# Performance work log

Measured on AMD Instinct MI355X. Metric: run time of the kernel, lower is better.

The kernel has to match this reference:

```python
import jax, jax.numpy as jnp
import numpy as np

D_MODEL = 1024
D_HEAD = 64
N_HEADS = D_MODEL // D_HEAD
MAX_SEQ = 2048
BATCH = 2
SEQ = 2048


def setup_inputs() -> dict:
    key = jax.random.key(0)
    ks = jax.random.split(key, 10)
    s = 1.0 / np.sqrt(D_MODEL)
    return {
        "x": jax.random.normal(ks[0], (BATCH, SEQ, D_MODEL), dtype=jnp.float32),
        "Wq": jax.random.normal(ks[1], (D_MODEL, D_MODEL), dtype=jnp.float32) * s,
        "bq": jax.random.normal(ks[2], (D_MODEL,), dtype=jnp.float32) * 0.01,
        "Wk": jax.random.normal(ks[3], (D_MODEL, D_MODEL), dtype=jnp.float32) * s,
        "bk": jax.random.normal(ks[4], (D_MODEL,), dtype=jnp.float32) * 0.01,
        "Wv": jax.random.normal(ks[5], (D_MODEL, D_MODEL), dtype=jnp.float32) * s,
        "bv": jax.random.normal(ks[6], (D_MODEL,), dtype=jnp.float32) * 0.01,
        "Er": jax.random.normal(ks[7], (MAX_SEQ, D_HEAD), dtype=jnp.float32),
        "Wo": jax.random.normal(ks[8], (D_MODEL, D_MODEL), dtype=jnp.float32) * s,
        "bo": jax.random.normal(ks[9], (D_MODEL,), dtype=jnp.float32) * 0.01,
    }


def _s_rel(q, Er):
    # q: [B,H,S,Dh]; use last S rows of Er (start = max_seq - seq)
    S = q.shape[2]
    Er_slice = Er[Er.shape[0] - S:, :]                  # [S, Dh]
    qE = jnp.einsum("bhsd,ld->bhsl", q, Er_slice)       # [B,H,S,S]
    padded = jnp.pad(qE, ((0, 0), (0, 0), (0, 0), (1, 0)))  # [B,H,S,S+1]
    B, H, S1, S2 = padded.shape
    padded = padded.reshape(B, H, S2, S1)               # skew trick
    return padded[:, :, 1:, :]                          # [B,H,S,S]


def reference(x, Wq, bq, Wk, bk, Wv, bv, Er, Wo, bo):
    B, S, _ = x.shape
    scale = 1.0 / np.sqrt(D_HEAD)
    # projections (torch Linear: x @ W.T + b)
    def proj(W, b):
        return (x @ W.T + b).reshape(B, S, N_HEADS, D_HEAD).transpose(0, 2, 1, 3)
    q = proj(Wq, bq)   # [B,H,S,Dh]
    k = proj(Wk, bk)
    v = proj(Wv, bv)
    qk = jnp.einsum("bhsd,bhtd->bhst", q, k)            # [B,H,S,S]
    logits = (qk + _s_rel(q, Er)) * scale
    causal = jnp.tril(jnp.ones((S, S), dtype=bool))
    masked = jnp.where(causal[None, None], logits, -1e9)
    attn = jax.nn.softmax(masked, axis=-1)
    out = jnp.einsum("bhst,bhtd->bhsd", attn, v)        # [B,H,S,Dh]
    out = out.transpose(0, 2, 1, 3).reshape(B, S, D_MODEL)
    return out @ Wo.T + bo
```

## Files before the change

### kernel.cpp

```cpp
#include <hip/hip_runtime.h>
#include <hip/hip_bf16.h>

typedef short v8s __attribute__((ext_vector_type(8)));
typedef float v4f __attribute__((ext_vector_type(4)));
typedef __hip_bfloat16 bf16;
typedef unsigned int u32;

#define MFMA(a, b, c) __builtin_amdgcn_mfma_f32_16x16x32_bf16(a, b, c, 0, 0, 0)

__device__ __forceinline__ void gload16(const bf16* g, bf16* l) {
    __builtin_amdgcn_global_load_lds(
        (const __attribute__((address_space(1))) u32*)(g),
        (__attribute__((address_space(3))) u32*)(l), 16, 0, 0);
}

__global__ __launch_bounds__(256) void cast_all(
    const float* __restrict__ x,  const float* __restrict__ wq,
    const float* __restrict__ wk, const float* __restrict__ wv,
    const float* __restrict__ wo, const float* __restrict__ er,
    bf16* __restrict__ xb,  bf16* __restrict__ wqb, bf16* __restrict__ wkb,
    bf16* __restrict__ wvb, bf16* __restrict__ wob, bf16* __restrict__ erb)
{
    const int r = blockIdx.y;
    const float* s; bf16* d; int n4;
    if      (r == 0) { s = x;  d = xb;  n4 = 1048576; }
    else if (r == 1) { s = wq; d = wqb; n4 = 262144;  }
    else if (r == 2) { s = wk; d = wkb; n4 = 262144;  }
    else if (r == 3) { s = wv; d = wvb; n4 = 262144;  }
    else if (r == 4) { s = wo; d = wob; n4 = 262144;  }
    else             { s = er; d = erb; n4 = 32768;   }
    const int i = blockIdx.x * 256 + threadIdx.x;
    if (i < n4) {
        const float4 v = ((const float4*)s)[i];
        bf16 t[4];
        t[0] = __float2bfloat16(v.x);
        t[1] = __float2bfloat16(v.y);
        t[2] = __float2bfloat16(v.z);
        t[3] = __float2bfloat16(v.w);
        ((uint2*)d)[i] = *(const uint2*)t;
    }
}

__global__ __launch_bounds__(256) void gemm_nt(
    const bf16* __restrict__ A, const bf16* __restrict__ W,
    const float* __restrict__ b0, const float* __restrict__ b1,
    const float* __restrict__ b2,
    bf16* __restrict__ oHM, bf16* __restrict__ Vt, float* __restrict__ outf)
{
    __shared__ bf16 As[128 * 64];
    __shared__ bf16 Bs[128 * 64];

    const int tid = threadIdx.x;
    const int w  = tid >> 6, l = tid & 63;
    const int lm = l & 15,  lq = l >> 4;
    const int wm = (w >> 1) * 64, wn = (w & 1) * 64;
    const int m0 = blockIdx.y * 128, n0 = blockIdx.x * 128;

    const int grow = l >> 3;
    const int gcol = ((l & 7) ^ grow) * 8;

    v4f acc[4][4];
#pragma unroll
    for (int i = 0; i < 4; ++i)
#pragma unroll
        for (int j = 0; j < 4; ++j) acc[i][j] = (v4f){0.f, 0.f, 0.f, 0.f};

    const int sw = (lm & 7) << 4;

    for (int k0 = 0; k0 < 1024; k0 += 64) {
        __syncthreads();
#pragma unroll
        for (int q = 0; q < 4; ++q) {
            const int rr = w * 32 + q * 8;
            gload16(&A[(size_t)(m0 + rr + grow) * 1024 + k0 + gcol], &As[rr * 64]);
            gload16(&W[(size_t)(n0 + rr + grow) * 1024 + k0 + gcol], &Bs[rr * 64]);
        }
        __syncthreads();
#pragma unroll
        for (int kk = 0; kk < 2; ++kk) {
            v8s a[4], b[4];
            const int cb = (lq * 16 + kk * 64);
#pragma unroll
            for (int i = 0; i < 4; ++i) {
                const int row = wm + i * 16 + lm;
                a[i] = *(const v8s*)((const char*)As + row * 128 + (cb ^ sw));
            }
#pragma unroll
            for (int j = 0; j < 4; ++j) {
                const int row = wn + j * 16 + lm;
                b[j] = *(const v8s*)((const char*)Bs + row * 128 + (cb ^ sw));
            }
#pragma unroll
            for (int i = 0; i < 4; ++i)
#pragma unroll
                for (int j = 0; j < 4; ++j)
                    acc[i][j] = MFMA(b[j], a[i], acc[i][j]);
        }
    }

    const int z = blockIdx.x >> 3;
    const float* bias = (z == 0) ? b0 : (z == 1) ? b1 : b2;

    float4 bj[4];
#pragma unroll
    for (int j = 0; j < 4; ++j)
        bj[j] = *(const float4*)&bias[(n0 & 1023) + wn + j * 16 + lq * 4];

#pragma unroll
    for (int i = 0; i < 4; ++i) {
        const int row = m0 + wm + i * 16 + lm;
        const int bb = row >> 11, ss = row & 2047;
#pragma unroll
        for (int j = 0; j < 4; ++j) {
            const int cc = (n0 & 1023) + wn + j * 16 + lq * 4;
            const float v0 = acc[i][j][0] + bj[j].x;
            const float v1 = acc[i][j][1] + bj[j].y;
            const float v2 = acc[i][j][2] + bj[j].z;
            const float v3 = acc[i][j][3] + bj[j].w;
            if (outf) {
                const float4 fv = {v0, v1, v2, v3};
                *(float4*)&outf[(size_t)row * 1024 + cc] = fv;
            } else {
                bf16 t[4];
                t[0] = __float2bfloat16(v0);
                t[1] = __float2bfloat16(v1);
                t[2] = __float2bfloat16(v2);
                t[3] = __float2bfloat16(v3);
                const int hh = cc >> 6, dd = cc & 63;
                if (z < 2) {
                    *(uint2*)&oHM[(size_t)z * 4194304 +
                        ((size_t)(bb * 16 + hh) * 2048 + ss) * 64 + dd] = *(uint2*)t;
                } else {
#pragma unroll
                    for (int r = 0; r < 4; ++r)
                        Vt[((size_t)(bb * 16 + hh) * 64 + dd + r) * 2048 + ss] = t[r];
                }
            }
        }
    }
}

__global__ __launch_bounds__(256, 5) void attn(
    const bf16* __restrict__ Q, const bf16* __restrict__ K,
    const bf16* __restrict__ Vt, const bf16* __restrict__ Er,
    bf16* __restrict__ AO, float* __restrict__ Opart, float* __restrict__ dpart)
{
    __shared__ bf16 Ks[64 * 72];
    __shared__ bf16 Vs[64 * 72];
    __shared__ bf16 GPs[64 * 84];

    const int ord = blockIdx.x;
    int bh, qb, t0, t1, slot = -1;
    if (ord < 960) {
        qb = 31 - (ord >> 6);
        const int sub = ord & 63;
        bh = sub >> 1;
        const int half = sub & 1;
        const int hh2 = (qb + 1) >> 1;
        t0 = half ? hh2 : 0;
        t1 = half ? (qb + 1) : hh2;
        slot = ((31 - qb) * 32 + bh) * 2 + half;
    } else {
        const int g2 = ord - 960;
        qb = 16 - (g2 >> 5);
        bh = g2 & 31;
        t0 = 0; t1 = qb + 1;
    }

    const int i0 = qb * 64;
    const int b  = bh >> 4, h = bh & 15;
    const int tid = threadIdx.x;
    const int w  = tid >> 6, l = tid & 63;
    const int lm = l & 15,  lq = l >> 4;

    const bf16* qp = Q + ((size_t)bh * 2048 + i0 + w * 16 + lm) * 64 + lq * 8;
    const v8s q0 = *(const v8s*)qp;
    const v8s q1f = *(const v8s*)(qp + 32);

    v4f accO[4];
#pragma unroll
    for (int dt = 0; dt < 4; ++dt) accO[dt] = (v4f){0.f, 0.f, 0.f, 0.f};
    float rs[4];
#pragma unroll
    for (int r = 0; r < 4; ++r) rs[r] = 0.f;

    const int sr0 = tid >> 3;
    const int sc8 = (tid & 7) * 8;
    const size_t kbase = (size_t)bh * 2048 * 64;
    const size_t vbase = (size_t)bh * 64 * 2048;

    const int jt0 = t0 * 64;
    uint4 kp0 = *(const uint4*)&K[kbase + (size_t)(jt0 + sr0) * 64 + sc8];
    uint4 kp1 = *(const uint4*)&K[kbase + (size_t)(jt0 + sr0 + 32) * 64 + sc8];
    uint4 vp0 = *(const uint4*)&Vt[vbase + (size_t)sr0 * 2048 + jt0 + sc8];
    uint4 vp1 = *(const uint4*)&Vt[vbase + (size_t)(sr0 + 32) * 2048 + jt0 + sc8];

    for (int it = t0; it < t1; ++it) {
        const int j0 = it * 64;
        __syncthreads();
        *(uint4*)&Ks[sr0 * 72 + sc8]        = kp0;
        *(uint4*)&Ks[(sr0 + 32) * 72 + sc8] = kp1;
        *(uint4*)&Vs[sr0 * 72 + sc8]        = vp0;
        *(uint4*)&Vs[(sr0 + 32) * 72 + sc8] = vp1;
        if (it + 1 < t1) {
            const int jn = j0 + 64;
            kp0 = *(const uint4*)&K[kbase + (size_t)(jn + sr0) * 64 + sc8];
            kp1 = *(const uint4*)&K[kbase + (size_t)(jn + sr0 + 32) * 64 + sc8];
            vp0 = *(const uint4*)&Vt[vbase + (size_t)sr0 * 2048 + jn + sc8];
            vp1 = *(const uint4*)&Vt[vbase + (size_t)(sr0 + 32) * 2048 + jn + sc8];
        }
        const int basew = 2048 - 16 - i0 + j0 - 16 * w;
#pragma unroll
        for (int ct2 = 0; ct2 < 5; ++ct2) {
            int mr = basew + ct2 * 16 + lm;
            mr = (mr > 2047) ? 2047 : mr;
            const bf16* ep = Er + (size_t)mr * 64 + lq * 8;
            const v8s e0 = *(const v8s*)ep;
            const v8s e1 = *(const v8s*)(ep + 32);
            v4f g = (v4f){0.f, 0.f, 0.f, 0.f};
            g = MFMA(q0, e0, g);
            g = MFMA(q1f, e1, g);
#pragma unroll
            for (int r = 0; r < 4; ++r)
                GPs[(w * 16 + lq * 4 + r) * 84 + ct2 * 16 + lm] =
                    __float2bfloat16(g[r] * 0.125f);
        }
        __syncthreads();
        v4f sv[4];
#pragma unroll
        for (int ct = 0; ct < 4; ++ct) {
            const v8s k0f = *(const v8s*)&Ks[(ct * 16 + lm) * 72 + lq * 8];
            const v8s k1f = *(const v8s*)&Ks[(ct * 16 + lm) * 72 + 32 + lq * 8];
            v4f s = (v4f){0.f, 0.f, 0.f, 0.f};
            s = MFMA(q0, k0f, s);
            s = MFMA(q1f, k1f, s);
            sv[ct] = s;
        }
#pragma unroll
        for (int r = 0; r < 4; ++r) {
            const int rl = lq * 4 + r;
            const int ig = i0 + w * 16 + rl;
#pragma unroll
            for (int ct = 0; ct < 4; ++ct) {
                const int jj = ct * 16 + lm;
                const float gb = (float)GPs[(w * 16 + rl) * 84 + jj + 15 - rl];
                float s = fmaf(sv[ct][r], 0.125f, gb);
                if (j0 + jj > ig) s = -1e9f;
                const float pe = __expf(s - 4.0f);
                rs[r] += pe;
                GPs[(w * 16 + rl) * 84 + jj] = __float2bfloat16(pe);
            }
        }
        const v8s pa0 = *(const v8s*)&GPs[(w * 16 + lm) * 84 + lq * 8];
        const v8s pa1 = *(const v8s*)&GPs[(w * 16 + lm) * 84 + 32 + lq * 8];
#pragma unroll
        for (int dt = 0; dt < 4; ++dt) {
            const v8s vb0 = *(const v8s*)&Vs[(dt * 16 + lm) * 72 + lq * 8];
            const v8s vb1 = *(const v8s*)&Vs[(dt * 16 + lm) * 72 + 32 + lq * 8];
            accO[dt] = MFMA(pa0, vb0, accO[dt]);
            accO[dt] = MFMA(pa1, vb1, accO[dt]);
        }
    }
#pragma unroll
    for (int r = 0; r < 4; ++r) {
#pragma unroll
        for (int msk = 8; msk >= 1; msk >>= 1)
            rs[r] += __shfl_xor(rs[r], msk, 64);
    }
    if (slot < 0) {
#pragma unroll
        for (int dt = 0; dt < 4; ++dt) {
#pragma unroll
            for (int r = 0; r < 4; ++r) {
                const int row = i0 + w * 16 + lq * 4 + r;
                const int d   = dt * 16 + lm;
                const float v = accO[dt][r] / rs[r];
                AO[((size_t)b * 2048 + row) * 1024 + h * 64 + d] = __float2bfloat16(v);
            }
        }
    } else {
        float* op = Opart + (size_t)slot * 4096;
#pragma unroll
        for (int dt = 0; dt < 4; ++dt) {
#pragma unroll
            for (int r = 0; r < 4; ++r) {
                const int row = w * 16 + lq * 4 + r;
                op[row * 64 + dt * 16 + lm] = accO[dt][r];
            }
        }
        if (lm == 0) {
#pragma unroll
            for (int r = 0; r < 4; ++r)
                dpart[slot * 64 + w * 16 + lq * 4 + r] = rs[r];
        }
    }
}

__global__ __launch_bounds__(256) void fixup(
    const float* __restrict__ Opart, const float* __restrict__ dpart,
    bf16* __restrict__ AO)
{
    const int pi = blockIdx.x;
    const int qb = 31 - (pi >> 5);
    const int bh = pi & 31;
    const int b = bh >> 4, h = bh & 15;
    const int t = threadIdx.x;
    const int row = t >> 2;
    const int c0 = (t & 3) * 16;
    const float dA = dpart[(pi * 2) * 64 + row];
    const float dB = dpart[(pi * 2 + 1) * 64 + row];
    const float inv = 1.0f / (dA + dB);
    const float* A = Opart + (size_t)(pi * 2) * 4096 + row * 64 + c0;
    const float* B = Opart + (size_t)(pi * 2 + 1) * 4096 + row * 64 + c0;
    bf16* dst = AO + ((size_t)b * 2048 + qb * 64 + row) * 1024 + h * 64 + c0;
#pragma unroll
    for (int c = 0; c < 16; c += 4) {
        bf16 tt[4];
#pragma unroll
        for (int r = 0; r < 4; ++r)
            tt[r] = __float2bfloat16((A[c + r] + B[c + r]) * inv);
        *(uint2*)&dst[c] = *(uint2*)tt;
    }
}

extern "C" void kernel_launch(void* const* d_in, const int* in_sizes, int n_in,
                              void* d_out, int out_size, void* d_ws, size_t ws_size,
                              hipStream_t stream)
{
    const float* x  = (const float*)d_in[0];
    const float* Wq = (const float*)d_in[1];
    const float* bq = (const float*)d_in[2];
    const float* Wk = (const float*)d_in[3];
    const float* bk = (const float*)d_in[4];
    const float* Wv = (const float*)d_in[5];
    const float* bv = (const float*)d_in[6];
    const float* Er = (const float*)d_in[7];
    const float* Wo = (const float*)d_in[8];
    const float* bo = (const float*)d_in[9];
    float* out = (float*)d_out;

    bf16* ws = (bf16*)d_ws;
    const size_t NEl = (size_t)4096 * 1024;
    bf16* Qw  = ws;
    bf16* Kw  = ws + NEl;
    bf16* Vtw = ws + 3 * NEl;
    bf16* xb  = ws + 4 * NEl;
    bf16* AOw = xb;
    bf16* Wqb = ws + 5 * NEl;
    bf16* Wkb = Wqb + 1024 * 1024;
    bf16* Wvb = Wkb + 1024 * 1024;
    bf16* Wob = Wvb + 1024 * 1024;
    bf16* Erb = Wob + 1024 * 1024;
    float* dpart = (float*)(Erb + (size_t)2048 * 64);
    float* Opart = out;
    (void)Kw;

    cast_all<<<dim3(4096, 6), 256, 0, stream>>>(x, Wq, Wk, Wv, Wo, Er,
                                                xb, Wqb, Wkb, Wvb, Wob, Erb);
    gemm_nt<<<dim3(24, 32), 256, 0, stream>>>(xb, Wqb, bq, bk, bv, Qw, Vtw, nullptr);
    attn<<<dim3(1504), 256, 0, stream>>>(Qw, Kw, Vtw, Erb, AOw, Opart, dpart);
    fixup<<<dim3(480), 256, 0, stream>>>(Opart, dpart, AOw);
    gemm_nt<<<dim3(8, 32), 256, 0, stream>>>(AOw, Wob, bo, bo, bo, nullptr, nullptr, out);
}
```

Measured before the change: 328.5 us.

## Double-buffer GEMM LDS tiles and rebalance attention work with interleaved KV splits

The GEMM now uses two LDS buffers so the global-to-LDS load of the next k-tile overlaps MFMA work on the current one, which also removes one barrier per iteration. The attention kernel replaces its contiguous half-splits with a table-driven schedule that splits query blocks 16-31 into even and odd KV tiles. Jobs are ordered so long and short work interleaves, and separate P and G LDS buffers remove aliasing. Occupancy is lowered to 4 blocks per SM because of the extra LDS, and the fixup kernel now covers 512 split blocks.

```diff
diff --git a/kernel.cpp b/kernel.cpp
--- a/kernel.cpp
+++ b/kernel.cpp
@@ -47,8 +47,8 @@
     const float* __restrict__ b2,
     bf16* __restrict__ oHM, bf16* __restrict__ Vt, float* __restrict__ outf)
 {
-    __shared__ bf16 As[128 * 64];
-    __shared__ bf16 Bs[128 * 64];
+    __shared__ bf16 As[2][128 * 64];
+    __shared__ bf16 Bs[2][128 * 64];
 
     const int tid = threadIdx.x;
     const int w  = tid >> 6, l = tid & 63;
@@ -67,15 +67,15 @@
 
     const int sw = (lm & 7) << 4;
 
-    for (int k0 = 0; k0 < 1024; k0 += 64) {
-        __syncthreads();
+    auto STAGE = [&](int p, int k0) {
 #pragma unroll
         for (int q = 0; q < 4; ++q) {
             const int rr = w * 32 + q * 8;
-            gload16(&A[(size_t)(m0 + rr + grow) * 1024 + k0 + gcol], &As[rr * 64]);
-            gload16(&W[(size_t)(n0 + rr + grow) * 1024 + k0 + gcol], &Bs[rr * 64]);
-        }
-        __syncthreads();
+            gload16(&A[(size_t)(m0 + rr + grow) * 1024 + k0 + gcol], &As[p][rr * 64]);
+            gload16(&W[(size_t)(n0 + rr + grow) * 1024 + k0 + gcol], &Bs[p][rr * 64]);
+        }
+    };
+    auto COMPUTE = [&](int p) {
 #pragma unroll
         for (int kk = 0; kk < 2; ++kk) {
             v8s a[4], b[4];
@@ -83,12 +83,12 @@
 #pragma unroll
             for (int i = 0; i < 4; ++i) {
                 const int row = wm + i * 16 + lm;
-                a[i] = *(const v8s*)((const char*)As + row * 128 + (cb ^ sw));
+                a[i] = *(const v8s*)((const char*)As[p] + row * 128 + (cb ^ sw));
             }
 #pragma unroll
             for (int j = 0; j < 4; ++j) {
                 const int row = wn + j * 16 + lm;
-                b[j] = *(const v8s*)((const char*)Bs + row * 128 + (cb ^ sw));
+                b[j] = *(const v8s*)((const char*)Bs[p] + row * 128 + (cb ^ sw));
             }
 #pragma unroll
             for (int i = 0; i < 4; ++i)
@@ -96,7 +96,16 @@
                 for (int j = 0; j < 4; ++j)
                     acc[i][j] = MFMA(b[j], a[i], acc[i][j]);
         }
-    }
+    };
+
+    STAGE(0, 0);
+    __syncthreads();
+    for (int t = 0; t < 15; ++t) {
+        STAGE((t + 1) & 1, (t + 1) * 64);
+        COMPUTE(t & 1);
+        __syncthreads();
+    }
+    COMPUTE(1);
 
     const int z = blockIdx.x >> 3;
     const float* bias = (z == 0) ? b0 : (z == 1) ? b1 : b2;
@@ -140,32 +149,33 @@
     }
 }
 
-__global__ __launch_bounds__(256, 5) void attn(
+__device__ const unsigned char QBt[48] = {
+    31,31,30,15, 30,29,29,28,14, 28,27,27,26,13, 26,25,25,24,12,
+    24,23,23,22,11, 22,21,21,20,10, 20,19,19,18,9, 18,17,17,16,8,
+    16,7, 6,5,4,3,2,1,0};
+__device__ const unsigned char TTt[48] = {
+     0, 1, 0, 2,  1, 0, 1, 0, 2,  1, 0, 1, 0, 2,  1, 0, 1, 0, 2,
+     1, 0, 1, 0, 2,  1, 0, 1, 0, 2,  1, 0, 1, 0, 2,  1, 0, 1, 0, 2,
+     1, 2, 2,2,2,2,2,2,2};
+
+__global__ __launch_bounds__(256, 4) void attn(
     const bf16* __restrict__ Q, const bf16* __restrict__ K,
     const bf16* __restrict__ Vt, const bf16* __restrict__ Er,
     bf16* __restrict__ AO, float* __restrict__ Opart, float* __restrict__ dpart)
 {
     __shared__ bf16 Ks[64 * 72];
     __shared__ bf16 Vs[64 * 72];
-    __shared__ bf16 GPs[64 * 84];
+    __shared__ bf16 Ps[64 * 72];
+    __shared__ bf16 Gs[64 * 84];
 
     const int ord = blockIdx.x;
-    int bh, qb, t0, t1, slot = -1;
-    if (ord < 960) {
-        qb = 31 - (ord >> 6);
-        const int sub = ord & 63;
-        bh = sub >> 1;
-        const int half = sub & 1;
-        const int hh2 = (qb + 1) >> 1;
-        t0 = half ? hh2 : 0;
-        t1 = half ? (qb + 1) : hh2;
-        slot = ((31 - qb) * 32 + bh) * 2 + half;
-    } else {
-        const int g2 = ord - 960;
-        qb = 16 - (g2 >> 5);
-        bh = g2 & 31;
-        t0 = 0; t1 = qb + 1;
-    }
+    const int bh = ord & 31;
+    const int s  = ord >> 5;
+    const int qb = QBt[s];
+    const int tt = TTt[s];
+    const int t0   = (tt == 2) ? 0 : tt;
+    const int step = (tt == 2) ? 1 : 2;
+    const int slot = (tt == 2) ? -1 : (((qb - 16) * 32 + bh) * 2 + tt);
 
     const int i0 = qb * 64;
     const int b  = bh >> 4, h = bh & 15;
@@ -195,15 +205,15 @@
     uint4 vp0 = *(const uint4*)&Vt[vbase + (size_t)sr0 * 2048 + jt0 + sc8];
     uint4 vp1 = *(const uint4*)&Vt[vbase + (size_t)(sr0 + 32) * 2048 + jt0 + sc8];
 
-    for (int it = t0; it < t1; ++it) {
+    for (int it = t0; it <= qb; it += step) {
         const int j0 = it * 64;
         __syncthreads();
         *(uint4*)&Ks[sr0 * 72 + sc8]        = kp0;
         *(uint4*)&Ks[(sr0 + 32) * 72 + sc8] = kp1;
         *(uint4*)&Vs[sr0 * 72 + sc8]        = vp0;
         *(uint4*)&Vs[(sr0 + 32) * 72 + sc8] = vp1;
-        if (it + 1 < t1) {
-            const int jn = j0 + 64;
+        if (it + step <= qb) {
+            const int jn = j0 + step * 64;
             kp0 = *(const uint4*)&K[kbase + (size_t)(jn + sr0) * 64 + sc8];
             kp1 = *(const uint4*)&K[kbase + (size_t)(jn + sr0 + 32) * 64 + sc8];
             vp0 = *(const uint4*)&Vt[vbase + (size_t)sr0 * 2048 + jn + sc8];
@@ -222,7 +232,7 @@
             g = MFMA(q1f, e1, g);
 #pragma unroll
             for (int r = 0; r < 4; ++r)
-                GPs[(w * 16 + lq * 4 + r) * 84 + ct2 * 16 + lm] =
+                Gs[(w * 16 + lq * 4 + r) * 84 + ct2 * 16 + lm] =
                     __float2bfloat16(g[r] * 0.125f);
         }
         __syncthreads();
@@ -231,10 +241,10 @@
         for (int ct = 0; ct < 4; ++ct) {
             const v8s k0f = *(const v8s*)&Ks[(ct * 16 + lm) * 72 + lq * 8];
             const v8s k1f = *(const v8s*)&Ks[(ct * 16 + lm) * 72 + 32 + lq * 8];
-            v4f s = (v4f){0.f, 0.f, 0.f, 0.f};
-            s = MFMA(q0, k0f, s);
-            s = MFMA(q1f, k1f, s);
-            sv[ct] = s;
+            v4f s2 = (v4f){0.f, 0.f, 0.f, 0.f};
+            s2 = MFMA(q0, k0f, s2);
+            s2 = MFMA(q1f, k1f, s2);
+            sv[ct] = s2;
         }
 #pragma unroll
         for (int r = 0; r < 4; ++r) {
@@ -243,16 +253,16 @@
 #pragma unroll
             for (int ct = 0; ct < 4; ++ct) {
                 const int jj = ct * 16 + lm;
-                const float gb = (float)GPs[(w * 16 + rl) * 84 + jj + 15 - rl];
-                float s = fmaf(sv[ct][r], 0.125f, gb);
-                if (j0 + jj > ig) s = -1e9f;
-                const float pe = __expf(s - 4.0f);
+                const float gb = (float)Gs[(w * 16 + rl) * 84 + jj + 15 - rl];
+                float sc = fmaf(sv[ct][r], 0.125f, gb);
+                if (j0 + jj > ig) sc = -1e9f;
+                const float pe = __expf(sc - 4.0f);
                 rs[r] += pe;
-                GPs[(w * 16 + rl) * 84 + jj] = __float2bfloat16(pe);
-            }
-        }
-        const v8s pa0 = *(const v8s*)&GPs[(w * 16 + lm) * 84 + lq * 8];
-        const v8s pa1 = *(const v8s*)&GPs[(w * 16 + lm) * 84 + 32 + lq * 8];
+                Ps[(w * 16 + rl) * 72 + jj] = __float2bfloat16(pe);
+            }
+        }
+        const v8s pa0 = *(const v8s*)&Ps[(w * 16 + lm) * 72 + lq * 8];
+        const v8s pa1 = *(const v8s*)&Ps[(w * 16 + lm) * 72 + 32 + lq * 8];
 #pragma unroll
         for (int dt = 0; dt < 4; ++dt) {
             const v8s vb0 = *(const v8s*)&Vs[(dt * 16 + lm) * 72 + lq * 8];
@@ -301,7 +311,7 @@
     bf16* __restrict__ AO)
 {
     const int pi = blockIdx.x;
-    const int qb = 31 - (pi >> 5);
+    const int qb = 16 + (pi >> 5);
     const int bh = pi & 31;
     const int b = bh >> 4, h = bh & 15;
     const int t = threadIdx.x;
@@ -358,7 +368,7 @@
     cast_all<<<dim3(4096, 6), 256, 0, stream>>>(x, Wq, Wk, Wv, Wo, Er,
                                                 xb, Wqb, Wkb, Wvb, Wob, Erb);
     gemm_nt<<<dim3(24, 32), 256, 0, stream>>>(xb, Wqb, bq, bk, bv, Qw, Vtw, nullptr);
-    attn<<<dim3(1504), 256, 0, stream>>>(Qw, Kw, Vtw, Erb, AOw, Opart, dpart);
-    fixup<<<dim3(480), 256, 0, stream>>>(Opart, dpart, AOw);
+    attn<<<dim3(1536), 256, 0, stream>>>(Qw, Kw, Vtw, Erb, AOw, Opart, dpart);
+    fixup<<<dim3(512), 256, 0, stream>>>(Opart, dpart, AOw);
     gemm_nt<<<dim3(8, 32), 256, 0, stream>>>(AOw, Wob, bo, bo, bo, nullptr, nullptr, out);
 }
```

After: 275.9 us. 1.19x faster.
